# Kernel optimization log

Measured on AMD Instinct MI355X. Metric: run time of the kernel, lower is better.

The kernel has to match this reference:

```python
import jax, jax.numpy as jnp
import numpy as np

N, E, F, H, L, G, O = 100000, 1600000, 128, 128, 4, 512, 10
BN_EPS = 1e-5


def setup_inputs() -> dict:
    key = jax.random.key(0)
    ks = jax.random.split(key, 12)
    x = jax.random.normal(ks[0], (N, F), dtype=jnp.float32)
    edge_index = jax.random.randint(ks[1], (2, E), 0, N, dtype=jnp.int32)
    batch = jnp.sort(jax.random.randint(ks[2], (N,), 0, G, dtype=jnp.int32))
    s = 1.0 / np.sqrt(H)
    # 4 GIN layers, input_dim == hidden_dim so params stack uniformly
    W1s = jax.random.uniform(ks[3], (L, F, H), jnp.float32, -s, s)
    b1s = jnp.zeros((L, H), jnp.float32)
    W2s = jax.random.uniform(ks[4], (L, H, H), jnp.float32, -s, s)
    b2s = jnp.zeros((L, H), jnp.float32)
    eps = jnp.zeros((L,), jnp.float32)  # learnable eps, init 0
    gammas = jnp.ones((L, H), jnp.float32)
    betas = jnp.zeros((L, H), jnp.float32)
    Din = F + L * H  # concatenated graph embedding dim
    so = 1.0 / np.sqrt(Din)
    Wout = jax.random.uniform(ks[5], (Din, O), jnp.float32, -so, so)
    bout = jnp.zeros((O,), jnp.float32)
    return {"x": x, "edge_index": edge_index, "batch": batch,
            "W1s": W1s, "b1s": b1s, "W2s": W2s, "b2s": b2s, "eps": eps,
            "gammas": gammas, "betas": betas, "Wout": Wout, "bout": bout}


def reference(x, edge_index, batch, W1s, b1s, W2s, b2s, eps, gammas, betas, Wout, bout):
    src, dst = edge_index[0], edge_index[1]
    n = x.shape[0]
    pooled = [jax.ops.segment_sum(x, batch, num_segments=G)]  # [G, F]
    h = x
    for l in range(W1s.shape[0]):
        # GINConv: MLP((1+eps)*h + sum_{j in N(i)} h_j)
        agg = jax.ops.segment_sum(h[src], dst, num_segments=n)  # [N, H]
        z = (1.0 + eps[l]) * h + agg
        z = jax.nn.relu(z @ W1s[l] + b1s[l]) @ W2s[l] + b2s[l]
        # BatchNorm1d (batch statistics, biased variance) + ReLU; dropout=identity (eval)
        mu = z.mean(axis=0)
        var = z.var(axis=0)
        z = (z - mu) * jax.lax.rsqrt(var + BN_EPS) * gammas[l] + betas[l]
        h = jax.nn.relu(z)
        pooled.append(jax.ops.segment_sum(h, batch, num_segments=G))  # [G, H]
    emb = jnp.concatenate(pooled, axis=1)  # [G, F + L*H]
    return emb @ Wout + bout  # [G, O]
```

## Files before the change

### kernel.cpp

```cpp
#include <hip/hip_runtime.h>
#include <hip/hip_bf16.h>

typedef __attribute__((ext_vector_type(8))) __bf16 bf16x8;
typedef __attribute__((ext_vector_type(4))) float f32x4;
typedef unsigned short u16;
typedef unsigned int u32;

constexpr int Nn = 100000;
constexpr int Ee = 1600000;
constexpr int Hd = 128;
constexpr int Ll = 4;
constexpr int Gg = 512;
constexpr int Oo = 10;
constexpr int Din = Hd + Ll * Hd;
constexpr int PSPLIT = 4;
constexpr int NBLK = (Nn + 127) / 128;
constexpr int AGG_BLKS = 2048;

constexpr int NB = 256;
constexpr int NPB = 392;
constexpr int BCAP = 8192;
constexpr int BATCH = 8192;
constexpr int NBATCH = (Ee + BATCH - 1) / BATCH;
constexpr int XCVT_BLKS = Nn * Hd / 8 / 256;
constexpr int WPREP_BLKS = Ll * 2 * Hd * Hd / 256;
constexpr float BN_EPS = 1e-5f;

__device__ __forceinline__ int swzb(int row, int bc) {
  return (row << 8) + (bc ^ ((row & 7) << 4));
}

__device__ __forceinline__ u16 f2bf(float f) {
  __hip_bfloat16 b = __float2bfloat16(f);
  u16 u;
  __builtin_memcpy(&u, &b, 2);
  return u;
}

__device__ __forceinline__ float bf2f(u32 u) { return __uint_as_float(u << 16); }

__device__ __forceinline__ int lower_bound_dev(const int* a, int n, int key) {
  int lo = 0, hi = n;
  while (lo < hi) { int mid = (lo + hi) >> 1; if (a[mid] < key) lo = mid + 1; else hi = mid; }
  return lo;
}

__device__ __forceinline__ void bn_param(const float* __restrict__ stats,
                                         const float* __restrict__ gammas,
                                         const float* __restrict__ betas,
                                         int prevL, int f, float& sc, float& sh) {
  const float invn = 1.0f / (float)Nn;
  float mu = stats[f] * invn;
  float var = stats[128 + f] * invn - mu * mu;
  sc = gammas[prevL * Hd + f] * rsqrtf(var + BN_EPS);
  sh = betas[prevL * Hd + f] - mu * sc;
}

__device__ __forceinline__ void gload_lds16(const void* g, void* l) {
  __builtin_amdgcn_global_load_lds((const __attribute__((address_space(1))) unsigned int*)g,
                                   (__attribute__((address_space(3))) unsigned int*)l, 16, 0, 0);
}

__global__ __launch_bounds__(256) void prep_kernel(const float* __restrict__ x, __hip_bfloat16* __restrict__ xb,
                                                   const float* __restrict__ W1s, const float* __restrict__ W2s,
                                                   __hip_bfloat16* __restrict__ wt,
                                                   int* __restrict__ gptr,
                                                   const int* __restrict__ batch, int* __restrict__ gb,
                                                   float* __restrict__ emb, float* __restrict__ statsAll) {
  int b = blockIdx.x;
  int tid = threadIdx.x;
  if (b < XCVT_BLKS) {
    int i = b * 256 + tid;
    f32x4 v0 = *(const f32x4*)(x + (size_t)i * 8);
    f32x4 v1 = *(const f32x4*)(x + (size_t)i * 8 + 4);
    uint4 o;
    o.x = (u32)f2bf(v0[0]) | ((u32)f2bf(v0[1]) << 16);
    o.y = (u32)f2bf(v0[2]) | ((u32)f2bf(v0[3]) << 16);
    o.z = (u32)f2bf(v1[0]) | ((u32)f2bf(v1[1]) << 16);
    o.w = (u32)f2bf(v1[2]) | ((u32)f2bf(v1[3]) << 16);
    *(uint4*)((u16*)xb + (size_t)i * 8) = o;
  } else if (b < XCVT_BLKS + WPREP_BLKS) {
    int idx = (b - XCVT_BLKS) * 256 + tid;
    int l = idx >> 15;
    int w = (idx >> 14) & 1;
    int nn = (idx >> 7) & 127;
    int k = idx & 127;
    const float* W = w ? W2s : W1s;
    wt[idx] = __float2bfloat16(W[l * Hd * Hd + k * Hd + nn]);
  } else if (b == XCVT_BLKS + WPREP_BLKS) {
    gptr[tid] = tid * BCAP;
    for (int g = tid; g <= Gg; g += 256)
      gb[g] = (g == Gg) ? Nn : lower_bound_dev(batch, Nn, g);
  } else {
    f32x4 z4 = (f32x4){0.f, 0.f, 0.f, 0.f};
    for (int i = tid; i < Gg * Din / 4; i += 256) ((f32x4*)emb)[i] = z4;
    for (int i = tid; i < Ll * 256; i += 256) statsAll[i] = 0.f;
  }
}

__global__ __launch_bounds__(256) void binA_kernel(const int* __restrict__ src, const int* __restrict__ dst,
                                                   int* __restrict__ gptr, u32* __restrict__ buckets) {
  __shared__ int hist[NB];
  __shared__ int lbase[NB];
  __shared__ int lpos[NB];
  __shared__ int gbaseS[NB];
  __shared__ int scanT[NB];
  __shared__ u32 reorder[BATCH];
  const int tid = threadIdx.x;
  const int e0 = blockIdx.x * BATCH;
  const int n = min(BATCH, Ee - e0);

  hist[tid] = 0;
  __syncthreads();
  for (int k = tid; k < n; k += 256) {
    int d = dst[e0 + k];
    atomicAdd(&hist[d / NPB], 1);
  }
  __syncthreads();
  int v = hist[tid];
  scanT[tid] = v;
  __syncthreads();
  for (int off = 1; off < NB; off <<= 1) {
    int x = (tid >= off) ? scanT[tid - off] : 0;
    __syncthreads();
    scanT[tid] += x;
    __syncthreads();
  }
  lbase[tid] = scanT[tid] - v;
  lpos[tid] = 0;
  __syncthreads();
  for (int k = tid; k < n; k += 256) {
    int d = dst[e0 + k];
    int s = src[e0 + k];
    int b = d / NPB;
    int dlo = d - b * NPB;
    int p = lbase[b] + atomicAdd(&lpos[b], 1);
    reorder[p] = ((u32)dlo << 17) | (u32)s;
  }
  __syncthreads();
  if (hist[tid] > 0) gbaseS[tid] = atomicAdd(&gptr[tid], hist[tid]);
  __syncthreads();
  for (int p = tid; p < n; p += 256) {
    int lo = 0, hi = NB - 1;
    while (lo < hi) { int mid = (lo + hi + 1) >> 1; if (lbase[mid] <= p) lo = mid; else hi = mid - 1; }
    buckets[gbaseS[lo] + (p - lbase[lo])] = reorder[p];
  }
}

__global__ __launch_bounds__(256) void bucketscan_kernel(const int* __restrict__ gptr,
                                                         int* __restrict__ bmeta,
                                                         int* __restrict__ indptr) {
  __shared__ int sc[NB];
  int tid = threadIdx.x;
  int cnt = gptr[tid] - tid * BCAP;
  sc[tid] = cnt;
  __syncthreads();
  for (int off = 1; off < NB; off <<= 1) {
    int x = (tid >= off) ? sc[tid - off] : 0;
    __syncthreads();
    sc[tid] += x;
    __syncthreads();
  }
  bmeta[tid] = cnt;
  bmeta[NB + tid] = sc[tid] - cnt;
  if (tid == 0) indptr[Nn] = Ee;
}

__global__ __launch_bounds__(512) void place_kernel(const u32* __restrict__ buckets,
                                                    const int* __restrict__ bmeta,
                                                    int* __restrict__ indptr, int* __restrict__ adj) {
  __shared__ int ncnt[512];
  __shared__ int nofs[NPB];
  __shared__ int lcur[NPB];
  const int tid = threadIdx.x;
  const int b = blockIdx.x;
  const int cnt = bmeta[b];
  const int adjbase = bmeta[NB + b];
  const int ebase = b * BCAP;
  const int node0 = b * NPB;
  const int nnodes = min(NPB, Nn - node0);

  ncnt[tid] = 0;
  if (tid < NPB) lcur[tid] = 0;
  __syncthreads();
  for (int k = tid; k < cnt; k += 512) atomicAdd(&ncnt[buckets[ebase + k] >> 17], 1);
  __syncthreads();
  int v = ncnt[tid];
  for (int off = 1; off < 512; off <<= 1) {
    int x = (tid >= off) ? ncnt[tid - off] : 0;
    __syncthreads();
    ncnt[tid] += x;
    __syncthreads();
  }
  if (tid < NPB) nofs[tid] = ncnt[tid] - v;
  __syncthreads();
  if (tid < nnodes) indptr[node0 + tid] = adjbase + nofs[tid];
  for (int k = tid; k < cnt; k += 512) {
    u32 u = buckets[ebase + k];
    int dlo = u >> 17;
    int s = (int)(u & 0x1FFFFu);
    int p = atomicAdd(&lcur[dlo], 1);
    adj[adjbase + nofs[dlo] + p] = s;
  }
}

__global__ __launch_bounds__(256) void agg_kernel(const __hip_bfloat16* __restrict__ zprev,
                                                  const int* __restrict__ indptr,
                                                  const int* __restrict__ adj,
                                                  const float* __restrict__ stats,
                                                  const float* __restrict__ gammas,
                                                  const float* __restrict__ betas,
                                                  const float* __restrict__ epsp,
                                                  int layer, float negLim,
                                                  __hip_bfloat16* __restrict__ t) {
  const int gwave = blockIdx.x * 4 + (threadIdx.x >> 6);
  const int nwaves = AGG_BLKS * 4;
  const int lane = threadIdx.x & 63;
  const int cb = lane * 2;
  const u16* zp = (const u16*)zprev;
  float sc0 = 1.f, sh0 = 0.f, sc1 = 1.f, sh1 = 0.f;
  if (layer > 0) {
    bn_param(stats, gammas, betas, layer - 1, cb, sc0, sh0);
    bn_param(stats, gammas, betas, layer - 1, cb + 1, sc1, sh1);
  }
  const float eps1 = 1.0f + epsp[layer];

  for (int node = gwave; node < Nn; node += nwaves) {
    int s = __builtin_amdgcn_readfirstlane(indptr[node]);
    int e = __builtin_amdgcn_readfirstlane(indptr[node + 1]);
    float a0 = 0.f, a1 = 0.f;
    int p = s;
    while (p + 16 <= e) {
      u32 v[16];
      #pragma unroll
      for (int j = 0; j < 16; ++j) v[j] = *(const u32*)(zp + (size_t)adj[p + j] * Hd + cb);
      #pragma unroll
      for (int j = 0; j < 16; ++j) {
        a0 += fmaxf(fmaf(bf2f(v[j] & 0xffffu), sc0, sh0), negLim);
        a1 += fmaxf(fmaf(bf2f(v[j] >> 16), sc1, sh1), negLim);
      }
      p += 16;
    }
    if (p + 8 <= e) {
      u32 v[8];
      #pragma unroll
      for (int j = 0; j < 8; ++j) v[j] = *(const u32*)(zp + (size_t)adj[p + j] * Hd + cb);
      #pragma unroll
      for (int j = 0; j < 8; ++j) {
        a0 += fmaxf(fmaf(bf2f(v[j] & 0xffffu), sc0, sh0), negLim);
        a1 += fmaxf(fmaf(bf2f(v[j] >> 16), sc1, sh1), negLim);
      }
      p += 8;
    }
    if (p + 4 <= e) {
      u32 v[4];
      #pragma unroll
      for (int j = 0; j < 4; ++j) v[j] = *(const u32*)(zp + (size_t)adj[p + j] * Hd + cb);
      #pragma unroll
      for (int j = 0; j < 4; ++j) {
        a0 += fmaxf(fmaf(bf2f(v[j] & 0xffffu), sc0, sh0), negLim);
        a1 += fmaxf(fmaf(bf2f(v[j] >> 16), sc1, sh1), negLim);
      }
      p += 4;
    }
    for (; p < e; ++p) {
      u32 v0 = *(const u32*)(zp + (size_t)adj[p] * Hd + cb);
      a0 += fmaxf(fmaf(bf2f(v0 & 0xffffu), sc0, sh0), negLim);
      a1 += fmaxf(fmaf(bf2f(v0 >> 16), sc1, sh1), negLim);
    }
    u32 sv = *(const u32*)(zp + (size_t)node * Hd + cb);
    float s0 = fmaxf(fmaf(bf2f(sv & 0xffffu), sc0, sh0), negLim);
    float s1 = fmaxf(fmaf(bf2f(sv >> 16), sc1, sh1), negLim);
    float t0 = eps1 * s0 + a0;
    float t1 = eps1 * s1 + a1;
    *(u32*)((u16*)t + (size_t)node * Hd + cb) = (u32)f2bf(t0) | ((u32)f2bf(t1) << 16);
  }
}

__global__ __launch_bounds__(256) void mlp_kernel(const __hip_bfloat16* __restrict__ t,
                                                  const __hip_bfloat16* __restrict__ w1t,
                                                  const __hip_bfloat16* __restrict__ w2t,
                                                  const float* __restrict__ b1,
                                                  const float* __restrict__ b2,
                                                  __hip_bfloat16* __restrict__ z,
                                                  float* __restrict__ stats) {
  __shared__ __align__(16) unsigned char sA[32 * 1024];
  __shared__ __align__(16) unsigned char sW[32 * 1024];
  const int tid = threadIdx.x;
  const int m0 = blockIdx.x * 128;
  const int lane = tid & 63;
  const int wave = tid >> 6;

  #pragma unroll
  for (int blk = 0; blk < 8; ++blk) {
    const int chunk = wave * 512 + blk * 64 + lane;
    const int row = chunk >> 4, pos = chunk & 15;
    const int spos = pos ^ (row & 7);
    void* ldst = sA + (size_t)(wave * 512 + blk * 64) * 16;
    void* ldstW = sW + (size_t)(wave * 512 + blk * 64) * 16;
    gload_lds16((const unsigned char*)w1t + row * 256 + spos * 16, ldstW);
    gload_lds16((const unsigned char*)t + (size_t)(m0 + row) * 256 + spos * 16, ldst);
  }
  __syncthreads();

  const int lrow = lane & 15;
  const int lkb = (lane >> 4) << 4;
  const int wm = wave * 32;
  const int crow = (lane >> 4) << 2;

  f32x4 acc[2][8];
  #pragma unroll
  for (int a = 0; a < 2; ++a) {
    #pragma unroll
    for (int b = 0; b < 8; ++b) acc[a][b] = (f32x4){0.f, 0.f, 0.f, 0.f};
  }

  #pragma unroll
  for (int kk = 0; kk < 4; ++kk) {
    const int kb2 = kk * 64 + lkb;
    bf16x8 a0 = *(const bf16x8*)(sA + swzb(wm + lrow, kb2));
    bf16x8 a1 = *(const bf16x8*)(sA + swzb(wm + 16 + lrow, kb2));
    #pragma unroll
    for (int nf = 0; nf < 8; ++nf) {
      bf16x8 bfr = *(const bf16x8*)(sW + swzb(nf * 16 + lrow, kb2));
      acc[0][nf] = __builtin_amdgcn_mfma_f32_16x16x32_bf16(a0, bfr, acc[0][nf], 0, 0, 0);
      acc[1][nf] = __builtin_amdgcn_mfma_f32_16x16x32_bf16(a1, bfr, acc[1][nf], 0, 0, 0);
    }
  }
  __syncthreads();

  #pragma unroll
  for (int blk = 0; blk < 8; ++blk) {
    const int chunk = wave * 512 + blk * 64 + lane;
    const int row = chunk >> 4, pos = chunk & 15;
    const int spos = pos ^ (row & 7);
    gload_lds16((const unsigned char*)w2t + row * 256 + spos * 16,
                sW + (size_t)(wave * 512 + blk * 64) * 16);
  }
  #pragma unroll
  for (int nf = 0; nf < 8; ++nf) {
    const int col = nf * 16 + lrow;
    const float bb = b1[col];
    #pragma unroll
    for (int mf = 0; mf < 2; ++mf) {
      #pragma unroll
      for (int j = 0; j < 4; ++j) {
        float v = acc[mf][nf][j] + bb;
        v = v > 0.f ? v : 0.f;
        int row = wm + mf * 16 + crow + j;
        *(u16*)(sA + swzb(row, col * 2)) = f2bf(v);
      }
    }
  }
  __syncthreads();

  f32x4 acc2[2][8];
  #pragma unroll
  for (int a = 0; a < 2; ++a) {
    #pragma unroll
    for (int b = 0; b < 8; ++b) acc2[a][b] = (f32x4){0.f, 0.f, 0.f, 0.f};
  }
  #pragma unroll
  for (int kk = 0; kk < 4; ++kk) {
    const int kb2 = kk * 64 + lkb;
    bf16x8 a0 = *(const bf16x8*)(sA + swzb(wm + lrow, kb2));
    bf16x8 a1 = *(const bf16x8*)(sA + swzb(wm + 16 + lrow, kb2));
    #pragma unroll
    for (int nf = 0; nf < 8; ++nf) {
      bf16x8 bfr = *(const bf16x8*)(sW + swzb(nf * 16 + lrow, kb2));
      acc2[0][nf] = __builtin_amdgcn_mfma_f32_16x16x32_bf16(a0, bfr, acc2[0][nf], 0, 0, 0);
      acc2[1][nf] = __builtin_amdgcn_mfma_f32_16x16x32_bf16(a1, bfr, acc2[1][nf], 0, 0, 0);
    }
  }
  __syncthreads();

  float* sred = (float*)sA;
  float* qred = (float*)(sA + 2048);
  u16* zp = (u16*)z;
  #pragma unroll
  for (int nf = 0; nf < 8; ++nf) {
    const int col = nf * 16 + lrow;
    const float bb = b2[col];
    float s = 0.f, q = 0.f;
    #pragma unroll
    for (int mf = 0; mf < 2; ++mf) {
      #pragma unroll
      for (int j = 0; j < 4; ++j) {
        int grow = m0 + wm + mf * 16 + crow + j;
        if (grow < Nn) {
          float v = acc2[mf][nf][j] + bb;
          zp[(size_t)grow * Hd + col] = f2bf(v);
          s += v; q += v * v;
        }
      }
    }
    s += __shfl_xor(s, 16, 64); s += __shfl_xor(s, 32, 64);
    q += __shfl_xor(q, 16, 64); q += __shfl_xor(q, 32, 64);
    if (lane < 16) { sred[wave * 128 + col] = s; qred[wave * 128 + col] = q; }
  }
  __syncthreads();
  if (tid < 128) {
    float a = sred[tid] + sred[128 + tid] + sred[256 + tid] + sred[384 + tid];
    atomicAdd(&stats[tid], a);
  } else {
    int c = tid - 128;
    float a = qred[c] + qred[128 + c] + qred[256 + c] + qred[384 + c];
    atomicAdd(&stats[128 + c], a);
  }
}

__global__ __launch_bounds__(128) void pool_all_kernel(const __hip_bfloat16* __restrict__ xb,
                                                       const __hip_bfloat16* __restrict__ z0,
                                                       const __hip_bfloat16* __restrict__ z1,
                                                       const __hip_bfloat16* __restrict__ z2,
                                                       const __hip_bfloat16* __restrict__ z3,
                                                       const float* __restrict__ statsAll,
                                                       const float* __restrict__ gammas,
                                                       const float* __restrict__ betas,
                                                       const int* __restrict__ gb,
                                                       float* __restrict__ emb) {
  const int b = blockIdx.x;
  const int s = b / (Gg * PSPLIT);
  const int rem = b % (Gg * PSPLIT);
  const int g = rem / PSPLIT, sp = rem % PSPLIT;
  const __hip_bfloat16* zsrc = (s == 0) ? xb : (s == 1) ? z0 : (s == 2) ? z1 : (s == 3) ? z2 : z3;
  const float negLim = (s == 0) ? -3.4e38f : 0.f;
  const int colOff = s * Hd;
  const int c2 = (threadIdx.x & 63) * 2;
  const int rh = threadIdx.x >> 6;
  float sc0 = 1.f, sh0 = 0.f, sc1 = 1.f, sh1 = 0.f;
  if (s > 0) {
    bn_param(statsAll + (size_t)(s - 1) * 256, gammas, betas, s - 1, c2, sc0, sh0);
    bn_param(statsAll + (size_t)(s - 1) * 256, gammas, betas, s - 1, c2 + 1, sc1, sh1);
  }
  const int lo = gb[g], hi = gb[g + 1];
  const int len = hi - lo;
  if (len <= 0) return;
  const int chunk = (len + PSPLIT - 1) / PSPLIT;
  const int rs = lo + sp * chunk;
  const int re = min(rs + chunk, hi);
  if (rs >= re) return;
  const u16* zp = (const u16*)zsrc;
  float a0 = 0.f, a1 = 0.f, b0 = 0.f, b1v = 0.f, d0 = 0.f, d1 = 0.f, e0 = 0.f, e1 = 0.f;
  int i = rs + rh;
  for (; i + 6 < re; i += 8) {
    u32 v0 = *(const u32*)(zp + (size_t)i * Hd + c2);
    u32 v1 = *(const u32*)(zp + (size_t)(i + 2) * Hd + c2);
    u32 v2 = *(const u32*)(zp + (size_t)(i + 4) * Hd + c2);
    u32 v3 = *(const u32*)(zp + (size_t)(i + 6) * Hd + c2);
    a0 += fmaxf(fmaf(bf2f(v0 & 0xffffu), sc0, sh0), negLim);
    a1 += fmaxf(fmaf(bf2f(v0 >> 16), sc1, sh1), negLim);
    b0 += fmaxf(fmaf(bf2f(v1 & 0xffffu), sc0, sh0), negLim);
    b1v += fmaxf(fmaf(bf2f(v1 >> 16), sc1, sh1), negLim);
    d0 += fmaxf(fmaf(bf2f(v2 & 0xffffu), sc0, sh0), negLim);
    d1 += fmaxf(fmaf(bf2f(v2 >> 16), sc1, sh1), negLim);
    e0 += fmaxf(fmaf(bf2f(v3 & 0xffffu), sc0, sh0), negLim);
    e1 += fmaxf(fmaf(bf2f(v3 >> 16), sc1, sh1), negLim);
  }
  for (; i < re; i += 2) {
    u32 v = *(const u32*)(zp + (size_t)i * Hd + c2);
    a0 += fmaxf(fmaf(bf2f(v & 0xffffu), sc0, sh0), negLim);
    a1 += fmaxf(fmaf(bf2f(v >> 16), sc1, sh1), negLim);
  }
  a0 += b0 + d0 + e0;
  a1 += b1v + d1 + e1;
  atomicAdd(&emb[g * Din + colOff + c2], a0);
  atomicAdd(&emb[g * Din + colOff + c2 + 1], a1);
}

__global__ __launch_bounds__(64) void out_kernel(const float* __restrict__ emb, const float* __restrict__ Wout,
                                                 const float* __restrict__ bout, float* __restrict__ out) {
  int g = blockIdx.x;
  int lane = threadIdx.x;
  float acc[Oo];
  #pragma unroll
  for (int o = 0; o < Oo; ++o) acc[o] = 0.f;
  for (int d = lane; d < Din; d += 64) {
    float ev = emb[g * Din + d];
    #pragma unroll
    for (int o = 0; o < Oo; ++o) acc[o] += ev * Wout[d * Oo + o];
  }
  #pragma unroll
  for (int off = 32; off > 0; off >>= 1) {
    #pragma unroll
    for (int o = 0; o < Oo; ++o) acc[o] += __shfl_down(acc[o], off, 64);
  }
  if (lane == 0) {
    #pragma unroll
    for (int o = 0; o < Oo; ++o) out[g * Oo + o] = acc[o] + bout[o];
  }
}

extern "C" void kernel_launch(void* const* d_in, const int* in_sizes, int n_in,
                              void* d_out, int out_size, void* d_ws, size_t ws_size,
                              hipStream_t stream) {
  (void)in_sizes; (void)n_in; (void)out_size;
  const float* x = (const float*)d_in[0];
  const int* ei = (const int*)d_in[1];
  const int* src = ei;
  const int* dst = ei + Ee;
  const int* batch = (const int*)d_in[2];
  const float* W1s = (const float*)d_in[3];
  const float* b1s = (const float*)d_in[4];
  const float* W2s = (const float*)d_in[5];
  const float* b2s = (const float*)d_in[6];
  const float* eps = (const float*)d_in[7];
  const float* gammas = (const float*)d_in[8];
  const float* betas = (const float*)d_in[9];
  const float* Wout = (const float*)d_in[10];
  const float* bout = (const float*)d_in[11];
  float* out = (float*)d_out;

  unsigned char* ws = (unsigned char*)d_ws;
  size_t off = 0;
  auto alloc = [&](size_t bytes) -> void* {
    void* p = ws + off;
    off = (off + bytes + 255) & ~size_t(255);
    return p;
  };
  __hip_bfloat16* xb = (__hip_bfloat16*)alloc((size_t)Nn * Hd * 2);
  __hip_bfloat16* z[Ll];
  for (int l = 0; l < Ll; ++l) z[l] = (__hip_bfloat16*)alloc((size_t)Nn * Hd * 2);
  __hip_bfloat16* t = (__hip_bfloat16*)alloc((size_t)Nn * Hd * 2);
  int* indptr = (int*)alloc((size_t)(Nn + 1) * 4);
  int* adj = (int*)alloc((size_t)Ee * 4);
  u32* buckets = (u32*)alloc((size_t)NB * BCAP * 4);
  int* gptr = (int*)alloc((size_t)NB * 4);
  int* bmeta = (int*)alloc((size_t)2 * NB * 4);
  int* gb = (int*)alloc((size_t)(Gg + 1) * 4);
  float* emb = (float*)alloc((size_t)Gg * Din * 4);
  float* statsAll = (float*)alloc((size_t)Ll * 256 * 4);
  __hip_bfloat16* wt = (__hip_bfloat16*)alloc((size_t)Ll * 2 * Hd * Hd * 2);
  if (off > ws_size) return;

  prep_kernel<<<XCVT_BLKS + WPREP_BLKS + 2, 256, 0, stream>>>(x, xb, W1s, W2s, wt, gptr,
                                                              batch, gb, emb, statsAll);

  binA_kernel<<<NBATCH, 256, 0, stream>>>(src, dst, gptr, buckets);
  bucketscan_kernel<<<1, NB, 0, stream>>>(gptr, bmeta, indptr);
  place_kernel<<<NB, 512, 0, stream>>>(buckets, bmeta, indptr, adj);

  const __hip_bfloat16* zprev = xb;
  for (int l = 0; l < Ll; ++l) {
    float negLim = (l == 0) ? -3.4e38f : 0.f;
    agg_kernel<<<AGG_BLKS, 256, 0, stream>>>(zprev, indptr, adj,
                                             statsAll + (size_t)(l > 0 ? l - 1 : 0) * 256,
                                             gammas, betas, eps, l, negLim, t);
    mlp_kernel<<<NBLK, 256, 0, stream>>>(
        t, wt + (size_t)l * 2 * Hd * Hd, wt + (size_t)l * 2 * Hd * Hd + Hd * Hd,
        b1s + l * Hd, b2s + l * Hd, z[l], statsAll + (size_t)l * 256);
    zprev = z[l];
  }

  pool_all_kernel<<<5 * Gg * PSPLIT, 128, 0, stream>>>(xb, z[0], z[1], z[2], z[3],
                                                       statsAll, gammas, betas, gb, emb);

  out_kernel<<<Gg, 64, 0, stream>>>(emb, Wout, bout, out);
}
```

Baseline: 528.7 us.

## Fuse pooling with output projection, fold bucket scan into place kernel, raise agg grid

The pooling kernel now multiplies its partial graph sums by Wout directly and atomically accumulates into the final output, which removes the emb buffer, its zeroing, and the separate out_kernel. The single-block bucket scan is recomputed redundantly inside every place_kernel block, which removes one launch. The aggregation grid is also enlarged from 2048 to 8192 blocks. This trades two launches and an intermediate buffer for more atomics on the small output and redundant scan work in each block. Because the output is built from float atomics, the summation order is no longer fixed.

Result: faster. 514.3 us (median of 2 runs) (-2.7%).

```diff
diff --git a/kernel.cpp b/kernel.cpp
--- a/kernel.cpp
+++ b/kernel.cpp
@@ -15,7 +15,7 @@
 constexpr int Din = Hd + Ll * Hd;
 constexpr int PSPLIT = 4;
 constexpr int NBLK = (Nn + 127) / 128;
-constexpr int AGG_BLKS = 2048;
+constexpr int AGG_BLKS = 8192;
 
 constexpr int NB = 256;
 constexpr int NPB = 392;
@@ -66,7 +66,7 @@
                                                    __hip_bfloat16* __restrict__ wt,
                                                    int* __restrict__ gptr,
                                                    const int* __restrict__ batch, int* __restrict__ gb,
-                                                   float* __restrict__ emb, float* __restrict__ statsAll) {
+                                                   float* __restrict__ out, float* __restrict__ statsAll) {
   int b = blockIdx.x;
   int tid = threadIdx.x;
   if (b < XCVT_BLKS) {
@@ -92,8 +92,7 @@
     for (int g = tid; g <= Gg; g += 256)
       gb[g] = (g == Gg) ? Nn : lower_bound_dev(batch, Nn, g);
   } else {
-    f32x4 z4 = (f32x4){0.f, 0.f, 0.f, 0.f};
-    for (int i = tid; i < Gg * Din / 4; i += 256) ((f32x4*)emb)[i] = z4;
+    for (int i = tid; i < Gg * Oo; i += 256) out[i] = 0.f;
     for (int i = tid; i < Ll * 256; i += 256) statsAll[i] = 0.f;
   }
 }
@@ -147,35 +146,32 @@
   }
 }
 
-__global__ __launch_bounds__(256) void bucketscan_kernel(const int* __restrict__ gptr,
-                                                         int* __restrict__ bmeta,
-                                                         int* __restrict__ indptr) {
-  __shared__ int sc[NB];
-  int tid = threadIdx.x;
-  int cnt = gptr[tid] - tid * BCAP;
-  sc[tid] = cnt;
-  __syncthreads();
-  for (int off = 1; off < NB; off <<= 1) {
-    int x = (tid >= off) ? sc[tid - off] : 0;
-    __syncthreads();
-    sc[tid] += x;
-    __syncthreads();
-  }
-  bmeta[tid] = cnt;
-  bmeta[NB + tid] = sc[tid] - cnt;
-  if (tid == 0) indptr[Nn] = Ee;
-}
-
 __global__ __launch_bounds__(512) void place_kernel(const u32* __restrict__ buckets,
-                                                    const int* __restrict__ bmeta,
+                                                    const int* __restrict__ gptr,
                                                     int* __restrict__ indptr, int* __restrict__ adj) {
+  __shared__ int cntS[NB];
+  __shared__ int scanS[NB];
   __shared__ int ncnt[512];
   __shared__ int nofs[NPB];
   __shared__ int lcur[NPB];
   const int tid = threadIdx.x;
   const int b = blockIdx.x;
-  const int cnt = bmeta[b];
-  const int adjbase = bmeta[NB + b];
+
+  if (tid < NB) {
+    int c = gptr[tid] - tid * BCAP;
+    cntS[tid] = c;
+    scanS[tid] = c;
+  }
+  __syncthreads();
+  for (int off = 1; off < NB; off <<= 1) {
+    int x = 0;
+    if (tid < NB && tid >= off) x = scanS[tid - off];
+    __syncthreads();
+    if (tid < NB) scanS[tid] += x;
+    __syncthreads();
+  }
+  const int cnt = cntS[b];
+  const int adjbase = scanS[b] - cnt;
   const int ebase = b * BCAP;
   const int node0 = b * NPB;
   const int nnodes = min(NPB, Nn - node0);
@@ -195,6 +191,7 @@
   if (tid < NPB) nofs[tid] = ncnt[tid] - v;
   __syncthreads();
   if (tid < nnodes) indptr[node0 + tid] = adjbase + nofs[tid];
+  if (tid == 0 && b == 0) indptr[Nn] = Ee;
   for (int k = tid; k < cnt; k += 512) {
     u32 u = buckets[ebase + k];
     int dlo = u >> 17;
@@ -409,7 +406,7 @@
   }
 }
 
-__global__ __launch_bounds__(128) void pool_all_kernel(const __hip_bfloat16* __restrict__ xb,
+__global__ __launch_bounds__(128) void pool_out_kernel(const __hip_bfloat16* __restrict__ xb,
                                                        const __hip_bfloat16* __restrict__ z0,
                                                        const __hip_bfloat16* __restrict__ z1,
                                                        const __hip_bfloat16* __restrict__ z2,
@@ -418,7 +415,9 @@
                                                        const float* __restrict__ gammas,
                                                        const float* __restrict__ betas,
                                                        const int* __restrict__ gb,
-                                                       float* __restrict__ emb) {
+                                                       const float* __restrict__ Wout,
+                                                       const float* __restrict__ bout,
+                                                       float* __restrict__ out) {
   const int b = blockIdx.x;
   const int s = b / (Gg * PSPLIT);
   const int rem = b % (Gg * PSPLIT);
@@ -428,6 +427,7 @@
   const int colOff = s * Hd;
   const int c2 = (threadIdx.x & 63) * 2;
   const int rh = threadIdx.x >> 6;
+  const int lane = threadIdx.x & 63;
   float sc0 = 1.f, sh0 = 0.f, sc1 = 1.f, sh1 = 0.f;
   if (s > 0) {
     bn_param(statsAll + (size_t)(s - 1) * 256, gammas, betas, s - 1, c2, sc0, sh0);
@@ -435,11 +435,9 @@
   }
   const int lo = gb[g], hi = gb[g + 1];
   const int len = hi - lo;
-  if (len <= 0) return;
   const int chunk = (len + PSPLIT - 1) / PSPLIT;
   const int rs = lo + sp * chunk;
   const int re = min(rs + chunk, hi);
-  if (rs >= re) return;
   const u16* zp = (const u16*)zsrc;
   float a0 = 0.f, a1 = 0.f, b0 = 0.f, b1v = 0.f, d0 = 0.f, d1 = 0.f, e0 = 0.f, e1 = 0.f;
   int i = rs + rh;
@@ -464,30 +462,26 @@
   }
   a0 += b0 + d0 + e0;
   a1 += b1v + d1 + e1;
-  atomicAdd(&emb[g * Din + colOff + c2], a0);
-  atomicAdd(&emb[g * Din + colOff + c2 + 1], a1);
-}
-
-__global__ __launch_bounds__(64) void out_kernel(const float* __restrict__ emb, const float* __restrict__ Wout,
-                                                 const float* __restrict__ bout, float* __restrict__ out) {
-  int g = blockIdx.x;
-  int lane = threadIdx.x;
-  float acc[Oo];
-  #pragma unroll
-  for (int o = 0; o < Oo; ++o) acc[o] = 0.f;
-  for (int d = lane; d < Din; d += 64) {
-    float ev = emb[g * Din + d];
-    #pragma unroll
-    for (int o = 0; o < Oo; ++o) acc[o] += ev * Wout[d * Oo + o];
-  }
+
+  float po[Oo];
+  #pragma unroll
+  for (int o = 0; o < Oo; ++o)
+    po[o] = a0 * Wout[(colOff + c2) * Oo + o] + a1 * Wout[(colOff + c2 + 1) * Oo + o];
   #pragma unroll
   for (int off = 32; off > 0; off >>= 1) {
     #pragma unroll
-    for (int o = 0; o < Oo; ++o) acc[o] += __shfl_down(acc[o], off, 64);
-  }
+    for (int o = 0; o < Oo; ++o) po[o] += __shfl_down(po[o], off, 64);
+  }
+  __shared__ float red[2][Oo];
   if (lane == 0) {
     #pragma unroll
-    for (int o = 0; o < Oo; ++o) out[g * Oo + o] = acc[o] + bout[o];
+    for (int o = 0; o < Oo; ++o) red[rh][o] = po[o];
+  }
+  __syncthreads();
+  if (threadIdx.x < Oo) {
+    float v = red[0][threadIdx.x] + red[1][threadIdx.x];
+    if (s == 0 && sp == 0) v += bout[threadIdx.x];
+    atomicAdd(&out[g * Oo + threadIdx.x], v);
   }
 }
 
@@ -526,19 +520,16 @@
   int* adj = (int*)alloc((size_t)Ee * 4);
   u32* buckets = (u32*)alloc((size_t)NB * BCAP * 4);
   int* gptr = (int*)alloc((size_t)NB * 4);
-  int* bmeta = (int*)alloc((size_t)2 * NB * 4);
   int* gb = (int*)alloc((size_t)(Gg + 1) * 4);
-  float* emb = (float*)alloc((size_t)Gg * Din * 4);
   float* statsAll = (float*)alloc((size_t)Ll * 256 * 4);
   __hip_bfloat16* wt = (__hip_bfloat16*)alloc((size_t)Ll * 2 * Hd * Hd * 2);
   if (off > ws_size) return;
 
   prep_kernel<<<XCVT_BLKS + WPREP_BLKS + 2, 256, 0, stream>>>(x, xb, W1s, W2s, wt, gptr,
-                                                              batch, gb, emb, statsAll);
+                                                              batch, gb, out, statsAll);
 
   binA_kernel<<<NBATCH, 256, 0, stream>>>(src, dst, gptr, buckets);
-  bucketscan_kernel<<<1, NB, 0, stream>>>(gptr, bmeta, indptr);
-  place_kernel<<<NB, 512, 0, stream>>>(buckets, bmeta, indptr, adj);
+  place_kernel<<<NB, 512, 0, stream>>>(buckets, gptr, indptr, adj);
 
   const __hip_bfloat16* zprev = xb;
   for (int l = 0; l < Ll; ++l) {
@@ -552,8 +543,7 @@
     zprev = z[l];
   }
 
-  pool_all_kernel<<<5 * Gg * PSPLIT, 128, 0, stream>>>(xb, z[0], z[1], z[2], z[3],
-                                                       statsAll, gammas, betas, gb, emb);
-
-  out_kernel<<<Gg, 64, 0, stream>>>(emb, Wout, bout, out);
-}
+  pool_out_kernel<<<5 * Gg * PSPLIT, 128, 0, stream>>>(xb, z[0], z[1], z[2], z[3],
+                                                       statsAll, gammas, betas, gb,
+                                                       Wout, bout, out);
+}
```
